# Optimization experiments

Measured on AMD Instinct MI355X. Metric: run time of the kernel, lower is better.

Reference implementation:

```python
import jax, jax.numpy as jnp
import numpy as np

HEADS = 16

def setup_inputs() -> dict:
    key = jax.random.key(0)
    ks = jax.random.split(key, 5)
    B, N, D = 2, 2048, 1024
    q = jax.random.normal(ks[0], (B, N, D), dtype=jnp.float32)
    kv = jax.random.normal(ks[1], (B, N, D), dtype=jnp.float32)
    # nn.Linear default init scale ~ 1/sqrt(fan_in); use scaled normals
    s = 1.0 / np.sqrt(D)
    Wq = jax.random.normal(ks[2], (D, D), dtype=jnp.float32) * s
    Wkv = jax.random.normal(ks[3], (D, 2 * D), dtype=jnp.float32) * s
    Wout = jax.random.normal(ks[4], (D, D), dtype=jnp.float32) * s
    return {"q": q, "kv": kv, "Wq": Wq, "Wkv": Wkv, "Wout": Wout}

def reference(q, kv, Wq, Wkv, Wout):
    B, N, D = q.shape
    H = HEADS
    Dh = D // H
    scale = Dh ** -0.5
    # projections (Linear, no bias); weights stored [in, out]
    qp = q @ Wq                      # [B,N,D]
    kvp = kv @ Wkv                   # [B,N,2D]
    kp, vp = kvp[..., :D], kvp[..., D:]
    def split_heads(t):
        return t.reshape(B, N, H, Dh).transpose(0, 2, 1, 3)  # [B,H,N,Dh]
    qh, kh, vh = split_heads(qp), split_heads(kp), split_heads(vp)
    dots = jnp.einsum('bhid,bhjd->bhij', qh, kh) * scale
    # attn_fn = softmax computed in float32, cast back to input dtype
    attn = jax.nn.softmax(dots.astype(jnp.float32), axis=-1).astype(dots.dtype)
    out = jnp.einsum('bhij,bhjd->bhid', attn, vh)
    out = out.transpose(0, 2, 1, 3).reshape(B, N, D)
    return out @ Wout
```

## Files before the change

### kernel.cpp

```cpp
#include <hip/hip_runtime.h>
#include <hip/hip_bf16.h>
#include <stdint.h>

using u16 = unsigned short;
using bf16x8 = __attribute__((ext_vector_type(8))) short;
using bf16x4 = __attribute__((ext_vector_type(4))) short;
using f32x4  = __attribute__((ext_vector_type(4))) float;

__device__ __forceinline__ u16 f2bf(float f) {
  union { float f; uint32_t u; } v; v.f = f;
  uint32_t u = v.u;
  u += 0x7fffu + ((u >> 16) & 1u);
  return (u16)(u >> 16);
}

#define GLOBAL_LOAD_LDS16(gp, lp) \
  __builtin_amdgcn_global_load_lds((const __attribute__((address_space(1))) unsigned int*)(gp), \
                                   (__attribute__((address_space(3))) unsigned int*)(lp), 16, 0, 0)

#define MFMA32(a, b, c) __builtin_amdgcn_mfma_f32_16x16x32_bf16(a, b, c, 0, 0, 0)
#define MFMA16(a, b, c) __builtin_amdgcn_mfma_f32_16x16x16bf16_1k(a, b, c, 0, 0, 0)

__global__ __launch_bounds__(256) void cast2_k(const float4* __restrict__ q,
                                               u16* __restrict__ q16,
                                               const float4* __restrict__ kv,
                                               u16* __restrict__ kv16) {
  int blk = blockIdx.x;
  const float4* in; u16* out; int i;
  if (blk < 4096) { in = q; out = q16; i = blk * 256 + threadIdx.x; }
  else { in = kv; out = kv16; i = (blk - 4096) * 256 + threadIdx.x; }
  float4 f = in[i];
  ushort4 o;
  o.x = f2bf(f.x); o.y = f2bf(f.y); o.z = f2bf(f.z); o.w = f2bf(f.w);
  *(ushort4*)(out + (size_t)i * 4) = o;
}

__global__ __launch_bounds__(256) void prep_w_k(const float* __restrict__ Wq,
                                                const float* __restrict__ Wkv,
                                                const float* __restrict__ Wout,
                                                u16* __restrict__ WqT, u16* __restrict__ WkvT,
                                                u16* __restrict__ WoutT, float qscale) {
  __shared__ float tile[32][33];
  int blk = blockIdx.x;
  const float* in; u16* out; float sc; int idx;
  if (blk < 1024)      { in = Wq;   out = WqT;   sc = qscale; idx = blk; }
  else if (blk < 3072) { in = Wkv;  out = WkvT;  sc = 1.0f;   idx = blk - 1024; }
  else                 { in = Wout; out = WoutT; sc = 1.0f;   idx = blk - 3072; }
  const int K = 1024;
  const int N = (blk >= 1024 && blk < 3072) ? 2048 : 1024;
  int bk = (idx & 31) * 32, bn = (idx >> 5) * 32;
  int tx = threadIdx.x & 31, ty = threadIdx.x >> 5;
#pragma unroll
  for (int i = 0; i < 4; i++) {
    int r = ty * 4 + i;
    tile[r][tx] = in[(size_t)(bk + r) * N + bn + tx];
  }
  __syncthreads();
#pragma unroll
  for (int i = 0; i < 4; i++) {
    int r = ty * 4 + i;
    out[(size_t)(bn + r) * K + bk + tx] = f2bf(tile[tx][r] * sc);
  }
}

template <int BM, bool OUT_F32>
__device__ __forceinline__ void gemm_body(u16* lA, u16* lB,
                                          const u16* __restrict__ A, const u16* __restrict__ BT,
                                          void* __restrict__ Cv, int N, int K, int bm, int bn) {
  const int tid = threadIdx.x;
  const int lane = tid & 63, wave = tid >> 6;
  const int l15 = lane & 15, quad = lane >> 4;
  constexpr int MI = BM / 32;
  const int wm = (wave >> 1) * (BM / 2), wn = (wave & 1) * 64;

  f32x4 acc[MI][4] = {};

  const u16* Abase = A + (size_t)bm * BM * K;
  const u16* Bbase = BT + (size_t)bn * 128 * K;
  const int r0 = tid >> 2, c8 = (tid & 3) * 8;

  u16* lAw = lA + wave * 512;
  u16* lBw = lB + wave * 512;

  for (int k0 = 0; k0 < K; k0 += 32) {
    const u16* Ag = Abase + k0 + (size_t)r0 * K + c8;
    const u16* Bg = Bbase + k0 + (size_t)r0 * K + c8;
#pragma unroll
    for (int t = 0; t < BM / 64; t++)
      GLOBAL_LOAD_LDS16(Ag + (size_t)(t * 64) * K, lAw + t * 2048);
#pragma unroll
    for (int t = 0; t < 2; t++)
      GLOBAL_LOAD_LDS16(Bg + (size_t)(t * 64) * K, lBw + t * 2048);
    __syncthreads();

    bf16x8 aF[MI], bF[4];
#pragma unroll
    for (int mi = 0; mi < MI; mi++)
      aF[mi] = *(const bf16x8*)&lA[(wm + mi * 16 + l15) * 32 + quad * 8];
#pragma unroll
    for (int ni = 0; ni < 4; ni++)
      bF[ni] = *(const bf16x8*)&lB[(wn + ni * 16 + l15) * 32 + quad * 8];
#pragma unroll
    for (int mi = 0; mi < MI; mi++)
#pragma unroll
      for (int ni = 0; ni < 4; ni++)
        acc[mi][ni] = MFMA32(aF[mi], bF[ni], acc[mi][ni]);
    __syncthreads();
  }

  const int col0 = bn * 128 + wn + l15;
  const int rowb = bm * BM + wm + quad * 4;
#pragma unroll
  for (int mi = 0; mi < MI; mi++) {
#pragma unroll
    for (int ni = 0; ni < 4; ni++) {
#pragma unroll
      for (int r = 0; r < 4; r++) {
        int row = rowb + mi * 16 + r;
        int col = col0 + ni * 16;
        float v = acc[mi][ni][r];
        if (OUT_F32) ((float*)Cv)[(size_t)row * N + col] = v;
        else         ((u16*)Cv)[(size_t)row * N + col] = f2bf(v);
      }
    }
  }
}

__global__ __launch_bounds__(256) void proj_k(const u16* __restrict__ q16, const u16* __restrict__ WqT,
                                              u16* __restrict__ qp,
                                              const u16* __restrict__ kv16, const u16* __restrict__ WkvT,
                                              u16* __restrict__ kvp) {
  __shared__ u16 lA[128 * 32];
  __shared__ u16 lB[128 * 32];
  int blk = blockIdx.x;
  if (blk < 256) gemm_body<128, false>(lA, lB, q16, WqT, qp, 1024, 1024, blk >> 3, blk & 7);
  else { int b2 = blk - 256; gemm_body<128, false>(lA, lB, kv16, WkvT, kvp, 2048, 1024, b2 >> 4, b2 & 15); }
}

__global__ __launch_bounds__(256) void gemm_out_k(const u16* __restrict__ A, const u16* __restrict__ BT,
                                                  float* __restrict__ C) {
  __shared__ u16 lA[64 * 32];
  __shared__ u16 lB[128 * 32];
  int blk = blockIdx.x;
  gemm_body<64, true>(lA, lB, A, BT, C, 1024, 1024, blk >> 3, blk & 7);
}

__global__ __launch_bounds__(256) void vt_k(const u16* __restrict__ kvp,
                                            u16* __restrict__ VT) {
  __shared__ u16 lT[64 * 64];
  const int jt = blockIdx.x & 31;
  const int bh = blockIdx.x >> 5;
  const int b = bh >> 4, h = bh & 15;
  const int j0 = jt * 64;
  const int u = threadIdx.x;
  const int su = u >> 3;
  const int sc = (u & 7) * 8;

#pragma unroll
  for (int t = 0; t < 2; t++) {
    int j = su + t * 32;
    int s = (j ^ (j >> 3)) & 7;
    uint4 vv = *(const uint4*)(kvp + (size_t)(b * 2048 + j0 + j) * 2048 + 1024 + h * 64 + sc);
    *(uint4*)&lT[j * 64 + (sc ^ (s << 3))] = vv;
  }
  __syncthreads();

  const int jg = u & 7;
#pragma unroll
  for (int t = 0; t < 2; t++) {
    int d = su + t * 32;
    u16 tmp[8];
#pragma unroll
    for (int i = 0; i < 8; i++) {
      int j = jg * 8 + i;
      int s = (j ^ (j >> 3)) & 7;
      tmp[i] = lT[j * 64 + (d ^ (s << 3))];
    }
    *(uint4*)(VT + ((size_t)bh * 64 + d) * 2048 + j0 + jg * 8) = *(const uint4*)tmp;
  }
}

__global__ __launch_bounds__(256) void flash_attn_k(const u16* __restrict__ qp,
                                                    const u16* __restrict__ kvp,
                                                    const u16* __restrict__ VT,
                                                    u16* __restrict__ attn_out) {
  const int NSEQ = 2048, D = 1024, LDKV = 2048;
  const int mtile = blockIdx.x & 31;
  const int bh = blockIdx.x >> 5;
  const int b = bh >> 4, h = bh & 15;
  const int tid = threadIdx.x;
  const int lane = tid & 63, wave = tid >> 6;
  const int quad = lane >> 4, l15 = lane & 15;

  __shared__ u16 lK[2][128 * 64];
  __shared__ u16 lV[2][64 * 128];

  const u16* Qb  = qp + (size_t)(b * NSEQ + mtile * 64) * D + h * 64;
  const u16* Kb  = kvp + (size_t)(b * NSEQ) * LDKV + h * 64;
  const u16* VTb = VT + (size_t)bh * 64 * 2048;

  bf16x8 qa[2];
#pragma unroll
  for (int ks = 0; ks < 2; ks++)
    qa[ks] = *(const bf16x8*)(Qb + (size_t)(wave * 16 + l15) * D + ks * 32 + quad * 8);

#define STAGE(sel, J0)                                                                   \
  {                                                                                      \
    _Pragma("unroll")                                                                    \
    for (int t = 0; t < 4; t++) {                                                        \
      int g = t * 256 + tid;                                                             \
      int jr = g >> 3;                                                                   \
      int c = (g & 7) ^ (jr & 7);                                                        \
      GLOBAL_LOAD_LDS16(Kb + (size_t)((J0) + jr) * LDKV + c * 8,                         \
                        &lK[sel][wave * 512 + t * 2048]);                                \
    }                                                                                    \
    _Pragma("unroll")                                                                    \
    for (int t = 0; t < 4; t++) {                                                        \
      int g = t * 256 + tid;                                                             \
      int d = g >> 4;                                                                    \
      int c = (g & 15) ^ (d & 7);                                                        \
      GLOBAL_LOAD_LDS16(VTb + (size_t)d * 2048 + (J0) + c * 8,                           \
                        &lV[sel][wave * 512 + t * 2048]);                                \
    }                                                                                    \
  }

  STAGE(0, 0);

  f32x4 oacc[4] = {};
  float rs = 0.f;

  for (int it = 0; it < 16; it++) {
    const int cur = it & 1;
    __syncthreads();
    if (it < 15) STAGE(cur ^ 1, (it + 1) * 128);

    const u16* lKc = lK[cur];
    const u16* lVc = lV[cur];
    f32x4 sacc[8] = {};
#pragma unroll
    for (int ks = 0; ks < 2; ks++)
#pragma unroll
      for (int ni = 0; ni < 8; ni++) {
        int p = ((ks * 4 + quad) ^ (l15 & 7)) * 8;
        bf16x8 kb = *(const bf16x8*)&lKc[(ni * 16 + l15) * 64 + p];
        sacc[ni] = MFMA32(kb, qa[ks], sacc[ni]);
      }

#pragma unroll
    for (int ni = 0; ni < 8; ni++) {
      float p0 = __builtin_amdgcn_exp2f(sacc[ni][0]);
      float p1 = __builtin_amdgcn_exp2f(sacc[ni][1]);
      float p2 = __builtin_amdgcn_exp2f(sacc[ni][2]);
      float p3 = __builtin_amdgcn_exp2f(sacc[ni][3]);
      rs += (p0 + p1) + (p2 + p3);
      union { uint32_t u[2]; bf16x4 v; } pa;
      __hip_bfloat162 w01 = __float22bfloat162_rn(float2{p0, p1});
      __hip_bfloat162 w23 = __float22bfloat162_rn(float2{p2, p3});
      pa.u[0] = *(uint32_t*)&w01;
      pa.u[1] = *(uint32_t*)&w23;
#pragma unroll
      for (int di = 0; di < 4; di++) {
        int p = (((2 * ni + (quad >> 1)) ^ (l15 & 7)) * 8) + (quad & 1) * 4;
        bf16x4 vb = *(const bf16x4*)&lVc[(di * 16 + l15) * 128 + p];
        oacc[di] = MFMA16(pa.v, vb, oacc[di]);
      }
    }
  }

  rs += __shfl_xor(rs, 16, 64);
  rs += __shfl_xor(rs, 32, 64);
  float inv = 1.0f / rs;
  float invq[4];
#pragma unroll
  for (int r = 0; r < 4; r++)
    invq[r] = __shfl(inv, (lane & 48) + ((lane >> 4) << 2) + r, 64);

  u16* Ob = attn_out + (size_t)(b * NSEQ + mtile * 64) * D + h * 64;
#pragma unroll
  for (int di = 0; di < 4; di++)
#pragma unroll
    for (int r = 0; r < 4; r++) {
      float v = oacc[di][r] * invq[r];
      Ob[(size_t)(wave * 16 + quad * 4 + r) * D + di * 16 + l15] = f2bf(v);
    }
}

extern "C" void kernel_launch(void* const* d_in, const int* in_sizes, int n_in,
                              void* d_out, int out_size, void* d_ws, size_t ws_size,
                              hipStream_t stream) {
  const float* q    = (const float*)d_in[0];
  const float* kv   = (const float*)d_in[1];
  const float* Wq   = (const float*)d_in[2];
  const float* Wkv  = (const float*)d_in[3];
  const float* Wout = (const float*)d_in[4];
  float* out = (float*)d_out;

  char* ws = (char*)d_ws;
  const size_t MB = 1024 * 1024;
  u16* q16   = (u16*)(ws + 0);
  u16* kv16  = (u16*)(ws + 8 * MB);
  u16* WqT   = (u16*)(ws + 16 * MB);
  u16* WkvT  = (u16*)(ws + 18 * MB);
  u16* WoutT = (u16*)(ws + 22 * MB);
  u16* qp    = (u16*)(ws + 24 * MB);
  u16* kvp   = (u16*)(ws + 32 * MB);
  u16* attn  = q16;
  u16* VT    = kv16;

  const float qscale = 0.125f * 1.44269504f;

  cast2_k<<<8192, 256, 0, stream>>>((const float4*)q, q16, (const float4*)kv, kv16);
  prep_w_k<<<4096, 256, 0, stream>>>(Wq, Wkv, Wout, WqT, WkvT, WoutT, qscale);

  proj_k<<<768, 256, 0, stream>>>(q16, WqT, qp, kv16, WkvT, kvp);
  vt_k<<<1024, 256, 0, stream>>>(kvp, VT);
  flash_attn_k<<<1024, 256, 0, stream>>>(qp, kvp, VT, attn);
  gemm_out_k<<<512, 256, 0, stream>>>(attn, WoutT, out);
}
```

Before: 224.9 us.

## Split flash attention waves across key halves and reuse K/V fragments across query subtiles

```diff
diff --git a/kernel.cpp b/kernel.cpp
--- a/kernel.cpp
+++ b/kernel.cpp
@@ -21,33 +21,32 @@
 #define MFMA32(a, b, c) __builtin_amdgcn_mfma_f32_16x16x32_bf16(a, b, c, 0, 0, 0)
 #define MFMA16(a, b, c) __builtin_amdgcn_mfma_f32_16x16x16bf16_1k(a, b, c, 0, 0, 0)
 
-__global__ __launch_bounds__(256) void cast2_k(const float4* __restrict__ q,
-                                               u16* __restrict__ q16,
-                                               const float4* __restrict__ kv,
-                                               u16* __restrict__ kv16) {
-  int blk = blockIdx.x;
-  const float4* in; u16* out; int i;
-  if (blk < 4096) { in = q; out = q16; i = blk * 256 + threadIdx.x; }
-  else { in = kv; out = kv16; i = (blk - 4096) * 256 + threadIdx.x; }
-  float4 f = in[i];
-  ushort4 o;
-  o.x = f2bf(f.x); o.y = f2bf(f.y); o.z = f2bf(f.z); o.w = f2bf(f.w);
-  *(ushort4*)(out + (size_t)i * 4) = o;
-}
-
-__global__ __launch_bounds__(256) void prep_w_k(const float* __restrict__ Wq,
-                                                const float* __restrict__ Wkv,
-                                                const float* __restrict__ Wout,
-                                                u16* __restrict__ WqT, u16* __restrict__ WkvT,
-                                                u16* __restrict__ WoutT, float qscale) {
+__global__ __launch_bounds__(256) void prep_k(const float4* __restrict__ q, u16* __restrict__ q16,
+                                              const float4* __restrict__ kv, u16* __restrict__ kv16,
+                                              const float* __restrict__ Wq,
+                                              const float* __restrict__ Wkv,
+                                              const float* __restrict__ Wout,
+                                              u16* __restrict__ WqT, u16* __restrict__ WkvT,
+                                              u16* __restrict__ WoutT, float qscale) {
   __shared__ float tile[32][33];
   int blk = blockIdx.x;
+  if (blk < 8192) {
+    const float4* in; u16* out; int i;
+    if (blk < 4096) { in = q; out = q16; i = blk * 256 + threadIdx.x; }
+    else { in = kv; out = kv16; i = (blk - 4096) * 256 + threadIdx.x; }
+    float4 f = in[i];
+    ushort4 o;
+    o.x = f2bf(f.x); o.y = f2bf(f.y); o.z = f2bf(f.z); o.w = f2bf(f.w);
+    *(ushort4*)(out + (size_t)i * 4) = o;
+    return;
+  }
+  int b2 = blk - 8192;
   const float* in; u16* out; float sc; int idx;
-  if (blk < 1024)      { in = Wq;   out = WqT;   sc = qscale; idx = blk; }
-  else if (blk < 3072) { in = Wkv;  out = WkvT;  sc = 1.0f;   idx = blk - 1024; }
-  else                 { in = Wout; out = WoutT; sc = 1.0f;   idx = blk - 3072; }
+  if (b2 < 1024)      { in = Wq;   out = WqT;   sc = qscale; idx = b2; }
+  else if (b2 < 3072) { in = Wkv;  out = WkvT;  sc = 1.0f;   idx = b2 - 1024; }
+  else                 { in = Wout; out = WoutT; sc = 1.0f;   idx = b2 - 3072; }
   const int K = 1024;
-  const int N = (blk >= 1024 && blk < 3072) ? 2048 : 1024;
+  const int N = (b2 >= 1024 && b2 < 3072) ? 2048 : 1024;
   int bk = (idx & 31) * 32, bn = (idx >> 5) * 32;
   int tx = threadIdx.x & 31, ty = threadIdx.x >> 5;
 #pragma unroll
@@ -191,6 +190,7 @@
   const int tid = threadIdx.x;
   const int lane = tid & 63, wave = tid >> 6;
   const int quad = lane >> 4, l15 = lane & 15;
+  const int kw = wave & 1, qw = wave >> 1;
 
   __shared__ u16 lK[2][128 * 64];
   __shared__ u16 lV[2][64 * 128];
@@ -199,10 +199,12 @@
   const u16* Kb  = kvp + (size_t)(b * NSEQ) * LDKV + h * 64;
   const u16* VTb = VT + (size_t)bh * 64 * 2048;
 
-  bf16x8 qa[2];
-#pragma unroll
-  for (int ks = 0; ks < 2; ks++)
-    qa[ks] = *(const bf16x8*)(Qb + (size_t)(wave * 16 + l15) * D + ks * 32 + quad * 8);
+  bf16x8 qa[2][2];
+#pragma unroll
+  for (int nq = 0; nq < 2; nq++)
+#pragma unroll
+    for (int ks = 0; ks < 2; ks++)
+      qa[nq][ks] = *(const bf16x8*)(Qb + (size_t)(qw * 32 + nq * 16 + l15) * D + ks * 32 + quad * 8);
 
 #define STAGE(sel, J0)                                                                   \
   {                                                                                      \
@@ -226,8 +228,8 @@
 
   STAGE(0, 0);
 
-  f32x4 oacc[4] = {};
-  float rs = 0.f;
+  f32x4 oacc[2][4] = {};
+  float rs[2] = {0.f, 0.f};
 
   for (int it = 0; it < 16; it++) {
     const int cur = it & 1;
@@ -236,53 +238,91 @@
 
     const u16* lKc = lK[cur];
     const u16* lVc = lV[cur];
-    f32x4 sacc[8] = {};
+
+    bf16x8 kb[2][4];
 #pragma unroll
     for (int ks = 0; ks < 2; ks++)
 #pragma unroll
-      for (int ni = 0; ni < 8; ni++) {
-        int p = ((ks * 4 + quad) ^ (l15 & 7)) * 8;
-        bf16x8 kb = *(const bf16x8*)&lKc[(ni * 16 + l15) * 64 + p];
-        sacc[ni] = MFMA32(kb, qa[ks], sacc[ni]);
+      for (int ni = 0; ni < 4; ni++)
+        kb[ks][ni] = *(const bf16x8*)&lKc[(kw * 64 + ni * 16 + l15) * 64 +
+                                          (((ks * 4 + quad) ^ (l15 & 7)) * 8)];
+    bf16x4 vb[4][4];
+#pragma unroll
+    for (int ni = 0; ni < 4; ni++)
+#pragma unroll
+      for (int di = 0; di < 4; di++)
+        vb[ni][di] = *(const bf16x4*)&lVc[(di * 16 + l15) * 128 +
+                                          ((kw * 8) | ((ni * 2 + (quad >> 1)) ^ (l15 & 7))) * 8 +
+                                          (quad & 1) * 4];
+
+#pragma unroll
+    for (int nq = 0; nq < 2; nq++) {
+      f32x4 sacc[4] = {};
+#pragma unroll
+      for (int ks = 0; ks < 2; ks++)
+#pragma unroll
+        for (int ni = 0; ni < 4; ni++)
+          sacc[ni] = MFMA32(kb[ks][ni], qa[nq][ks], sacc[ni]);
+
+#pragma unroll
+      for (int ni = 0; ni < 4; ni++) {
+        float p0 = __builtin_amdgcn_exp2f(sacc[ni][0]);
+        float p1 = __builtin_amdgcn_exp2f(sacc[ni][1]);
+        float p2 = __builtin_amdgcn_exp2f(sacc[ni][2]);
+        float p3 = __builtin_amdgcn_exp2f(sacc[ni][3]);
+        rs[nq] += (p0 + p1) + (p2 + p3);
+        union { uint32_t u[2]; bf16x4 v; } pa;
+        __hip_bfloat162 w01 = __float22bfloat162_rn(float2{p0, p1});
+        __hip_bfloat162 w23 = __float22bfloat162_rn(float2{p2, p3});
+        pa.u[0] = *(uint32_t*)&w01;
+        pa.u[1] = *(uint32_t*)&w23;
+#pragma unroll
+        for (int di = 0; di < 4; di++)
+          oacc[nq][di] = MFMA16(pa.v, vb[ni][di], oacc[nq][di]);
       }
-
-#pragma unroll
-    for (int ni = 0; ni < 8; ni++) {
-      float p0 = __builtin_amdgcn_exp2f(sacc[ni][0]);
-      float p1 = __builtin_amdgcn_exp2f(sacc[ni][1]);
-      float p2 = __builtin_amdgcn_exp2f(sacc[ni][2]);
-      float p3 = __builtin_amdgcn_exp2f(sacc[ni][3]);
-      rs += (p0 + p1) + (p2 + p3);
-      union { uint32_t u[2]; bf16x4 v; } pa;
-      __hip_bfloat162 w01 = __float22bfloat162_rn(float2{p0, p1});
-      __hip_bfloat162 w23 = __float22bfloat162_rn(float2{p2, p3});
-      pa.u[0] = *(uint32_t*)&w01;
-      pa.u[1] = *(uint32_t*)&w23;
-#pragma unroll
-      for (int di = 0; di < 4; di++) {
-        int p = (((2 * ni + (quad >> 1)) ^ (l15 & 7)) * 8) + (quad & 1) * 4;
-        bf16x4 vb = *(const bf16x4*)&lVc[(di * 16 + l15) * 128 + p];
-        oacc[di] = MFMA16(pa.v, vb, oacc[di]);
-      }
-    }
-  }
-
-  rs += __shfl_xor(rs, 16, 64);
-  rs += __shfl_xor(rs, 32, 64);
-  float inv = 1.0f / rs;
-  float invq[4];
-#pragma unroll
-  for (int r = 0; r < 4; r++)
-    invq[r] = __shfl(inv, (lane & 48) + ((lane >> 4) << 2) + r, 64);
-
-  u16* Ob = attn_out + (size_t)(b * NSEQ + mtile * 64) * D + h * 64;
-#pragma unroll
-  for (int di = 0; di < 4; di++)
-#pragma unroll
-    for (int r = 0; r < 4; r++) {
-      float v = oacc[di][r] * invq[r];
-      Ob[(size_t)(wave * 16 + quad * 4 + r) * D + di * 16 + l15] = f2bf(v);
-    }
+    }
+  }
+
+#pragma unroll
+  for (int nq = 0; nq < 2; nq++) {
+    rs[nq] += __shfl_xor(rs[nq], 16, 64);
+    rs[nq] += __shfl_xor(rs[nq], 32, 64);
+  }
+
+  float* cb = (float*)lK;
+  float* rb = (float*)lV;
+  if (kw == 1) {
+#pragma unroll
+    for (int nq = 0; nq < 2; nq++) {
+#pragma unroll
+      for (int di = 0; di < 4; di++)
+#pragma unroll
+        for (int r = 0; r < 4; r++)
+          cb[((qw * 2 + nq) * 4 + di) * 256 + (quad * 4 + r) * 16 + l15] = oacc[nq][di][r];
+      if (quad == 0) rb[(qw * 2 + nq) * 16 + l15] = rs[nq];
+    }
+  }
+  __syncthreads();
+  if (kw == 0) {
+    u16* Ob = attn_out + (size_t)(b * NSEQ + mtile * 64) * D + h * 64;
+#pragma unroll
+    for (int nq = 0; nq < 2; nq++) {
+      rs[nq] += rb[(qw * 2 + nq) * 16 + l15];
+      float inv = 1.0f / rs[nq];
+      float invq[4];
+#pragma unroll
+      for (int r = 0; r < 4; r++)
+        invq[r] = __shfl(inv, (lane & 48) + ((lane >> 4) << 2) + r, 64);
+#pragma unroll
+      for (int di = 0; di < 4; di++)
+#pragma unroll
+        for (int r = 0; r < 4; r++) {
+          float v = (oacc[nq][di][r] +
+                     cb[((qw * 2 + nq) * 4 + di) * 256 + (quad * 4 + r) * 16 + l15]) * invq[r];
+          Ob[(size_t)(qw * 32 + nq * 16 + quad * 4 + r) * D + di * 16 + l15] = f2bf(v);
+        }
+    }
+  }
 }
 
 extern "C" void kernel_launch(void* const* d_in, const int* in_sizes, int n_in,
@@ -309,9 +349,8 @@
 
   const float qscale = 0.125f * 1.44269504f;
 
-  cast2_k<<<8192, 256, 0, stream>>>((const float4*)q, q16, (const float4*)kv, kv16);
-  prep_w_k<<<4096, 256, 0, stream>>>(Wq, Wkv, Wout, WqT, WkvT, WoutT, qscale);
-
+  prep_k<<<12288, 256, 0, stream>>>((const float4*)q, q16, (const float4*)kv, kv16,
+                                    Wq, Wkv, Wout, WqT, WkvT, WoutT, qscale);
   proj_k<<<768, 256, 0, stream>>>(q16, WqT, qp, kv16, WkvT, kvp);
   vt_k<<<1024, 256, 0, stream>>>(kvp, VT);
   flash_attn_k<<<1024, 256, 0, stream>>>(qp, kvp, VT, attn);
```

New measurement: 221.3 us. No clear change (-1.6%).
